# Kernel optimization log

Hardware: AMD Instinct MI355X
Metric: run time of the kernel (lower is better)

The kernel has to match this reference:

```python
import jax, jax.numpy as jnp
import numpy as np

N, F, H, C, E = 100000, 128, 64, 16, 1000000


def _prop(x, src, dst, w):
    # gather source features, scale by edge weight, scatter-add to destinations
    msgs = x[src] * w[:, None]  # [E, H]
    return jax.ops.segment_sum(msgs, dst, num_segments=N)


def _gru(x, h, W_ih, W_hh, b_ih, b_hh):
    gi = x @ W_ih.T + b_ih  # [N, 3H]
    gh = h @ W_hh.T + b_hh
    i_r, i_z, i_n = jnp.split(gi, 3, axis=1)
    h_r, h_z, h_n = jnp.split(gh, 3, axis=1)
    r = jax.nn.sigmoid(i_r + h_r)
    z = jax.nn.sigmoid(i_z + h_z)
    n = jnp.tanh(i_n + r * h_n)
    return (1.0 - z) * n + z * h


def setup_inputs() -> dict:
    key = jax.random.key(0)
    ks = jax.random.split(key, 20)
    s = 0.05
    inp = {
        'x': jax.random.normal(ks[0], (N, F), jnp.float32),
        'edge_index': jax.random.randint(ks[1], (2, E), 0, N),
        'edge_weight': jax.random.uniform(ks[2], (E,), jnp.float32),
        'edge_index_re': jax.random.randint(ks[3], (2, E), 0, N),
        'edge_weight_re': jax.random.uniform(ks[4], (E,), jnp.float32),
        'W_first': jax.random.normal(ks[5], (H, F), jnp.float32) * s,
        'b_first': jnp.zeros((H,), jnp.float32),
        'W_con1': jax.random.normal(ks[6], (H, 2 * H), jnp.float32) * s,
        'b_con1': jnp.zeros((H,), jnp.float32),
        'W_con2': jax.random.normal(ks[7], (H, 2 * H), jnp.float32) * s,
        'b_con2': jnp.zeros((H,), jnp.float32),
        'W_lin1': jax.random.normal(ks[8], (H, H), jnp.float32) * s,
        'b_lin1': jnp.zeros((H,), jnp.float32),
        'W_out': jax.random.normal(ks[9], (C, H), jnp.float32) * s,
        'b_out': jnp.zeros((C,), jnp.float32),
        'W_ih': jax.random.normal(ks[10], (3 * H, H), jnp.float32) * s,
        'W_hh': jax.random.normal(ks[11], (3 * H, H), jnp.float32) * s,
        'b_ih': jnp.zeros((3 * H,), jnp.float32),
        'b_hh': jnp.zeros((3 * H,), jnp.float32),
    }
    return inp


def reference(x, edge_index, edge_weight, edge_index_re, edge_weight_re,
              W_first, b_first, W_con1, b_con1, W_con2, b_con2,
              W_lin1, b_lin1, W_out, b_out, W_ih, W_hh, b_ih, b_hh):
    src, dst = edge_index[0], edge_index[1]
    src_r, dst_r = edge_index_re[0], edge_index_re[1]

    x = x @ W_first.T + b_first  # [N, H]; dropout is identity at inference
    h = x

    x1 = _prop(x, src, dst, edge_weight)
    x2 = _prop(x, src_r, dst_r, edge_weight_re)
    x = jnp.concatenate([x1, x2], axis=1) @ W_con1.T + b_con1
    x = _gru(x, h, W_ih, W_hh, b_ih, b_hh)
    x = x @ W_lin1.T + b_lin1

    x1 = _prop(x, src, dst, edge_weight)
    x2 = _prop(x, src_r, dst_r, edge_weight_re)
    x = jnp.concatenate([x1, x2], axis=1) @ W_con2.T + b_con2
    x = _gru(x, h, W_ih, W_hh, b_ih, b_hh)
    x = x @ W_out.T + b_out
    return jax.nn.log_softmax(x, axis=-1)
```

## Files before the change

### kernel.cpp

```cpp
#include <hip/hip_runtime.h>

#define NN 100000
#define FF 128
#define HH 64
#define CC 16
#define EE 1000000
#define NSEG (2*NN)
#define BSH 11
#define BKD  (1 << BSH)
#define NBUK ((NSEG + BKD - 1) / BKD)
#define EPB 4096
#define P1BLK ((2*EE + EPB - 1) / EPB)

typedef __bf16 bf16;
typedef __attribute__((ext_vector_type(8))) __bf16 bf16x8;
typedef __attribute__((ext_vector_type(4))) __bf16 bf16x4;
typedef __attribute__((ext_vector_type(4))) float f32x4;
typedef __attribute__((ext_vector_type(2))) float f32x2;

__device__ __forceinline__ float fsig(float t)  { return 1.0f/(1.0f+__expf(-t)); }
__device__ __forceinline__ float ftanh(float t) { return 1.0f - 2.0f/(__expf(2.0f*t)+1.0f); }

__device__ __forceinline__ unsigned pack_sw(int s, float w) {
    unsigned short u = __builtin_bit_cast(unsigned short, (bf16)w);
    return ((unsigned)s << 15) | (u & 0x7FFFu);
}

__global__ void precomp_kernel(const float* __restrict__ W_ih, const float* __restrict__ b_ih,
                               const float* __restrict__ Wc1,  const float* __restrict__ bc1,
                               const float* __restrict__ Wc2,  const float* __restrict__ bc2,
                               const float* __restrict__ W_hh, const float* __restrict__ W_first,
                               const float* __restrict__ W_lin1, const float* __restrict__ W_out,
                               bf16* __restrict__ W1bf, float* __restrict__ b1,
                               bf16* __restrict__ W2bf, float* __restrict__ b2,
                               bf16* __restrict__ Whbf, bf16* __restrict__ Wfbf,
                               bf16* __restrict__ Wlbf, bf16* __restrict__ Wobf)
{
    int idx = blockIdx.x*blockDim.x + threadIdx.x;
    const int t0 = 192*128;
    const int t1 = t0 + 192;
    const int t2 = t1 + 192*64;
    const int t3 = t2 + 64*128;
    const int t4 = t3 + 64*64;
    const int t5 = t4 + 16*64;
    if (idx < t0) {
        int j = idx >> 7, k = idx & 127;
        float s1 = 0.f, s2 = 0.f;
        for (int m=0; m<64; ++m) {
            float wih = W_ih[j*64+m];
            s1 += wih * Wc1[m*128+k];
            s2 += wih * Wc2[m*128+k];
        }
        W1bf[idx] = (bf16)s1; W2bf[idx] = (bf16)s2;
    } else if (idx < t1) {
        int j = idx - t0;
        float s1 = b_ih[j], s2 = b_ih[j];
        for (int m=0; m<64; ++m) {
            float wih = W_ih[j*64+m];
            s1 += wih * bc1[m];
            s2 += wih * bc2[m];
        }
        b1[j] = s1; b2[j] = s2;
    } else if (idx < t2) {
        int i = idx - t1;  Whbf[i] = (bf16)W_hh[i];
    } else if (idx < t3) {
        int i = idx - t2;  Wfbf[i] = (bf16)W_first[i];
    } else if (idx < t4) {
        int i = idx - t3;  Wlbf[i] = (bf16)W_lin1[i];
    } else if (idx < t5) {
        int i = idx - t4;  Wobf[i] = (bf16)W_out[i];
    }
}


__global__ __launch_bounds__(256) void bucket_count_kernel(const int* __restrict__ ei,
                                                           const int* __restrict__ ei_re,
                                                           int* __restrict__ bkcnt)
{
    __shared__ int hist[NBUK];
    const int t = threadIdx.x;
    for (int i=t; i<NBUK; i+=256) hist[i] = 0;
    __syncthreads();
    const long e0 = (long)blockIdx.x * EPB;
    #pragma unroll
    for (int it=0; it<16; ++it) {
        long e = e0 + it*256 + t;
        int d = -1;
        if (e < EE)        d = ei[EE + e];
        else if (e < 2*EE) d = NN + ei_re[EE + (e - EE)];
        if (d >= 0) atomicAdd(&hist[d >> BSH], 1);
    }
    __syncthreads();
    for (int i=t; i<NBUK; i+=256) if (hist[i]) atomicAdd(&bkcnt[i], hist[i]);
}

__global__ void bucket_scan_kernel(const int* __restrict__ bkcnt,
                                   int* __restrict__ bkbase, int* __restrict__ bkcur,
                                   int* __restrict__ rp)
{
    if (threadIdx.x == 0) {
        int acc = 0;
        for (int i=0; i<NBUK; ++i) { bkbase[i] = acc; bkcur[i] = acc; acc += bkcnt[i]; }
        bkbase[NBUK] = acc;
        rp[NSEG] = 2*EE;
    }
}

__global__ __launch_bounds__(256) void fillA_kernel(const int* __restrict__ ei,
                                                    const float* __restrict__ ew,
                                                    const int* __restrict__ ei_re,
                                                    const float* __restrict__ ew_re,
                                                    int* __restrict__ bkcur,
                                                    int* __restrict__ tmp_d,
                                                    unsigned* __restrict__ tmp_p)
{
    __shared__ int hist[NBUK];
    __shared__ int base[NBUK];
    const int t = threadIdx.x;
    for (int i=t; i<NBUK; i+=256) hist[i] = 0;
    __syncthreads();
    const long e0 = (long)blockIdx.x * EPB;
    int pr[16];
    #pragma unroll
    for (int it=0; it<16; ++it) {
        long e = e0 + it*256 + t;
        int d = -1;
        if (e < EE)        d = ei[EE + e];
        else if (e < 2*EE) d = NN + ei_re[EE + (e - EE)];
        if (d >= 0) {
            int b = d >> BSH;
            int r = atomicAdd(&hist[b], 1);
            pr[it] = (b << 16) | r;
        } else pr[it] = -1;
    }
    __syncthreads();
    for (int i=t; i<NBUK; i+=256) base[i] = atomicAdd(&bkcur[i], hist[i]);
    __syncthreads();
    #pragma unroll
    for (int it=0; it<16; ++it) {
        if (pr[it] < 0) continue;
        long e = e0 + it*256 + t;
        int d, s; float w;
        if (e < EE) { d = ei[EE+e]; s = ei[e]; w = ew[e]; }
        else { long j = e - EE; d = NN + ei_re[EE+j]; s = ei_re[j]; w = ew_re[j]; }
        int pos = base[pr[it] >> 16] + (pr[it] & 0xFFFF);
        tmp_d[pos] = d;
        tmp_p[pos] = pack_sw(s, w);
    }
}

__global__ __launch_bounds__(1024) void fillB_kernel(const int* __restrict__ bkbase,
                                                     const int* __restrict__ tmp_d,
                                                     const unsigned* __restrict__ tmp_p,
                                                     unsigned* __restrict__ edata,
                                                     int* __restrict__ rp)
{
    __shared__ int cntL[BKD];
    __shared__ int scanL[1024];
    const int t  = threadIdx.x;
    const int b  = blockIdx.x;
    const int d0 = b << BSH;
    const int dn = min(BKD, NSEG - d0);
    const int p0 = bkbase[b];
    const int p1 = bkbase[b+1];
    for (int i=t; i<BKD; i+=1024) cntL[i] = 0;
    __syncthreads();
    for (int pos = p0 + t; pos < p1; pos += 1024)
        atomicAdd(&cntL[tmp_d[pos] - d0], 1);
    __syncthreads();
    int a0 = cntL[2*t], a1 = cntL[2*t+1];
    int ps = a0 + a1;
    scanL[t] = ps;
    __syncthreads();
    #pragma unroll
    for (int off=1; off<1024; off<<=1) {
        int x = (t>=off) ? scanL[t-off] : 0;
        __syncthreads();
        scanL[t] += x;
        __syncthreads();
    }
    int g0 = p0 + scanL[t] - ps;
    int g1 = g0 + a0;
    if (2*t   < dn) rp[d0 + 2*t]   = g0;
    if (2*t+1 < dn) rp[d0 + 2*t+1] = g1;
    cntL[2*t]   = g0;
    cntL[2*t+1] = g1;
    __syncthreads();
    for (int pos = p0 + t; pos < p1; pos += 1024) {
        int d = tmp_d[pos];
        int p = atomicAdd(&cntL[d - d0], 1);
        edata[p] = tmp_p[pos];
    }
}

__global__ __launch_bounds__(256) void csr_prop_kernel(const bf16* __restrict__ X,
    const int* __restrict__ rp, const unsigned* __restrict__ edata,
    bf16* __restrict__ x1, bf16* __restrict__ x2)
{
    int s = blockIdx.x*4 + (threadIdx.x>>6);
    if (s >= NSEG) return;
    const int lane = threadIdx.x & 63;
    const int q  = lane >> 4;
    const int fl = lane & 15;
    const unsigned foff = 8u*(unsigned)fl;
    const int e0 = rp[s], e1 = rp[s+1];
    const char* Xb = (const char*)X;
    const char* Eb = (const char*)edata;

    f32x2 acc01 = {0.f, 0.f}, acc23 = {0.f, 0.f};
    int eq = e0 + q;
    unsigned eqb = 4u*(unsigned)eq;
    for (int base = e0; base < e1; base += 16, eq += 16, eqb += 64u) {
        const int rem = e1 - eq;
        #pragma unroll
        for (int j=0; j<4; ++j) {
            unsigned p = *(const unsigned*)(Eb + (eqb + 16u*(unsigned)j));
            const bool v = (4*j < rem);
            float w = v ? __uint_as_float((p & 0x7FFFu) << 16) : 0.f;
            unsigned voff = v ? (((p >> 8) & 0xFFFFFF80u) | foff) : foff;
            uint2 d = *(const uint2*)(Xb + voff);
            f32x2 lo = { __uint_as_float(d.x << 16), __uint_as_float(d.x & 0xFFFF0000u) };
            f32x2 hi = { __uint_as_float(d.y << 16), __uint_as_float(d.y & 0xFFFF0000u) };
            f32x2 w2 = { w, w };
            acc01 += w2 * lo;
            acc23 += w2 * hi;
        }
    }
    float a0 = acc01.x, a1 = acc01.y, a2 = acc23.x, a3 = acc23.y;
    a0 += __shfl_xor(a0, 32); a0 += __shfl_xor(a0, 16);
    a1 += __shfl_xor(a1, 32); a1 += __shfl_xor(a1, 16);
    a2 += __shfl_xor(a2, 32); a2 += __shfl_xor(a2, 16);
    a3 += __shfl_xor(a3, 32); a3 += __shfl_xor(a3, 16);
    if (q == 0) {
        bf16* o = (s < NN) ? &x1[(long)s*HH] : &x2[(long)(s-NN)*HH];
        bf16x4 ov = {(bf16)a0, (bf16)a1, (bf16)a2, (bf16)a3};
        *(bf16x4*)&o[4*fl] = ov;
    }
}


__global__ __launch_bounds__(256, 2) void lin_first_mfma_kernel(
    const float* __restrict__ X, const bf16* __restrict__ Wf,
    const float* __restrict__ b, float* __restrict__ Y, bf16* __restrict__ Ybf)
{
    const int t = threadIdx.x;
    const int w = t >> 6, lane = t & 63, col = lane & 15, quad = lane >> 4;
    bf16x8 B[4];
    #pragma unroll
    for (int ks=0; ks<4; ++ks)
        B[ks] = *(const bf16x8*)&Wf[(16*w+col)*128 + ks*32 + quad*8];
    const float bv = b[16*w + col];
    __shared__ bf16 Alds[32][136];
    const int m_st = t >> 3, c_in = t & 7;
    for (int tb = blockIdx.x*32; tb < NN; tb += gridDim.x*32) {
        const float4* rx = (const float4*)&X[(long)(tb+m_st)*FF];
        #pragma unroll
        for (int it=0; it<4; ++it) {
            int cc = c_in + it*8;
            float4 v = rx[cc];
            bf16x4 bvv = {(bf16)v.x,(bf16)v.y,(bf16)v.z,(bf16)v.w};
            *(bf16x4*)&Alds[m_st][cc*4] = bvv;
        }
        __syncthreads();
        f32x4 acc[2] = {{0.f,0.f,0.f,0.f},{0.f,0.f,0.f,0.f}};
        #pragma unroll
        for (int ks=0; ks<4; ++ks)
            #pragma unroll
            for (int mt=0; mt<2; ++mt) {
                bf16x8 a = *(const bf16x8*)&Alds[mt*16+col][ks*32+quad*8];
                acc[mt] = __builtin_amdgcn_mfma_f32_16x16x32_bf16(a, B[ks], acc[mt], 0,0,0);
            }
        __syncthreads();
        #pragma unroll
        for (int mt=0; mt<2; ++mt)
            #pragma unroll
            for (int r=0; r<4; ++r) {
                long n = tb + mt*16 + quad*4 + r;
                float val = acc[mt][r] + bv;
                Y  [n*HH + 16*w+col] = val;
                Ybf[n*HH + 16*w+col] = (bf16)val;
            }
    }
}

template<int MODE>
__global__ __launch_bounds__(256, 2) void layer_fused_kernel(
    const bf16* __restrict__ X1, const bf16* __restrict__ X2,
    const float* __restrict__ H,
    const bf16* __restrict__ Wg, const float* __restrict__ bg,
    const bf16* __restrict__ Wh, const float* __restrict__ bh,
    const bf16* __restrict__ Ws, const float* __restrict__ bs,
    bf16* __restrict__ Obf, float* __restrict__ Of)
{
    const int t    = threadIdx.x;
    const int w    = t >> 6;
    const int lane = t & 63;
    const int col  = lane & 15;
    const int quad = lane >> 4;

    bf16x8 Bg[3][4];
    bf16x8 Bh[3][2];
    float bgv[3], bhv[3];
    #pragma unroll
    for (int jt=0; jt<3; ++jt) {
        int J = jt*64 + 16*w + col;
        #pragma unroll
        for (int ks=0; ks<4; ++ks)
            Bg[jt][ks] = *(const bf16x8*)&Wg[J*128 + ks*32 + quad*8];
        #pragma unroll
        for (int ks=0; ks<2; ++ks)
            Bh[jt][ks] = *(const bf16x8*)&Wh[J*64 + ks*32 + quad*8];
        bgv[jt] = bg[J];
        bhv[jt] = bh[J];
    }

    bf16x8 B2[2];
    float b2s;
    if constexpr (MODE == 0) {
        #pragma unroll
        for (int ks=0; ks<2; ++ks)
            B2[ks] = *(const bf16x8*)&Ws[(16*w+col)*64 + ks*32 + quad*8];
        b2s = bs[16*w + col];
    } else {
        #pragma unroll
        for (int ks=0; ks<2; ++ks)
            B2[ks] = *(const bf16x8*)&Ws[col*64 + ks*32 + quad*8];
        b2s = bs[col];
    }

    __shared__ bf16 Alds[32][200];
    __shared__ bf16 Glds[32][72];

    const int m_st = t >> 3;
    const int c_in = t & 7;

    for (int tb = blockIdx.x*32; tb < NN; tb += gridDim.x*32) {
        {
            long n = tb + m_st;
            *(bf16x8*)&Alds[m_st][c_in*8]      = *(const bf16x8*)&X1[n*HH + c_in*8];
            *(bf16x8*)&Alds[m_st][64 + c_in*8] = *(const bf16x8*)&X2[n*HH + c_in*8];
            const float4* rh = (const float4*)&H[n*HH];
            float4 a = rh[c_in*2], b4 = rh[c_in*2+1];
            bf16x8 hb = {(bf16)a.x,(bf16)a.y,(bf16)a.z,(bf16)a.w,
                         (bf16)b4.x,(bf16)b4.y,(bf16)b4.z,(bf16)b4.w};
            *(bf16x8*)&Alds[m_st][128 + c_in*8] = hb;
        }
        __syncthreads();

        f32x4 accg[2][3];
        f32x4 acch[2][3];
        #pragma unroll
        for (int mt=0; mt<2; ++mt)
            #pragma unroll
            for (int jt=0; jt<3; ++jt) {
                accg[mt][jt] = (f32x4){0.f,0.f,0.f,0.f};
                acch[mt][jt] = (f32x4){0.f,0.f,0.f,0.f};
            }

        #pragma unroll
        for (int ks=0; ks<4; ++ks) {
            #pragma unroll
            for (int mt=0; mt<2; ++mt) {
                bf16x8 a = *(const bf16x8*)&Alds[mt*16 + col][ks*32 + quad*8];
                #pragma unroll
                for (int jt=0; jt<3; ++jt)
                    accg[mt][jt] = __builtin_amdgcn_mfma_f32_16x16x32_bf16(
                        a, Bg[jt][ks], accg[mt][jt], 0, 0, 0);
            }
        }
        #pragma unroll
        for (int ks=0; ks<2; ++ks) {
            #pragma unroll
            for (int mt=0; mt<2; ++mt) {
                bf16x8 a = *(const bf16x8*)&Alds[mt*16 + col][128 + ks*32 + quad*8];
                #pragma unroll
                for (int jt=0; jt<3; ++jt)
                    acch[mt][jt] = __builtin_amdgcn_mfma_f32_16x16x32_bf16(
                        a, Bh[jt][ks], acch[mt][jt], 0, 0, 0);
            }
        }

        const int c = 16*w + col;
        #pragma unroll
        for (int mt=0; mt<2; ++mt) {
            #pragma unroll
            for (int r=0; r<4; ++r) {
                long n = tb + mt*16 + quad*4 + r;
                float gr = accg[mt][0][r] + bgv[0];
                float gz = accg[mt][1][r] + bgv[1];
                float gn = accg[mt][2][r] + bgv[2];
                float hr = acch[mt][0][r] + bhv[0];
                float hz = acch[mt][1][r] + bhv[1];
                float hn = acch[mt][2][r] + bhv[2];
                float rr = fsig(gr + hr);
                float zz = fsig(gz + hz);
                float nv = ftanh(gn + rr*hn);
                float hv = H[n*HH + c];
                Glds[mt*16 + quad*4 + r][c] = (bf16)((1.0f - zz)*nv + zz*hv);
            }
        }
        __syncthreads();

        if constexpr (MODE == 0) {
            f32x4 acc2[2] = {{0.f,0.f,0.f,0.f},{0.f,0.f,0.f,0.f}};
            #pragma unroll
            for (int ks=0; ks<2; ++ks)
                #pragma unroll
                for (int mt=0; mt<2; ++mt) {
                    bf16x8 a = *(const bf16x8*)&Glds[mt*16+col][ks*32+quad*8];
                    acc2[mt] = __builtin_amdgcn_mfma_f32_16x16x32_bf16(a, B2[ks], acc2[mt], 0,0,0);
                }
            #pragma unroll
            for (int mt=0; mt<2; ++mt)
                #pragma unroll
                for (int r=0; r<4; ++r)
                    Obf[(long)(tb+mt*16+quad*4+r)*HH + 16*w+col] = (bf16)(acc2[mt][r] + b2s);
        } else {
            if (w < 2) {
                f32x4 acc2 = {0.f,0.f,0.f,0.f};
                #pragma unroll
                for (int ks=0; ks<2; ++ks) {
                    bf16x8 a = *(const bf16x8*)&Glds[w*16+col][ks*32+quad*8];
                    acc2 = __builtin_amdgcn_mfma_f32_16x16x32_bf16(a, B2[ks], acc2, 0,0,0);
                }
                #pragma unroll
                for (int r=0; r<4; ++r) {
                    long n = tb + w*16 + quad*4 + r;
                    float val = acc2[r] + b2s;
                    float m = val;
                    #pragma unroll
                    for (int off=8; off>0; off>>=1) m = fmaxf(m, __shfl_xor(m, off, 16));
                    float ex = __expf(val - m);
                    float ssum = ex;
                    #pragma unroll
                    for (int off=8; off>0; off>>=1) ssum += __shfl_xor(ssum, off, 16);
                    Of[n*CC + col] = val - m - __logf(ssum);
                }
            }
        }
    }
}

extern "C" void kernel_launch(void* const* d_in, const int* in_sizes, int n_in,
                              void* d_out, int out_size, void* d_ws, size_t ws_size,
                              hipStream_t stream)
{
    const float* x       = (const float*)d_in[0];
    const int*   ei      = (const int*)  d_in[1];
    const float* ew      = (const float*)d_in[2];
    const int*   ei_re   = (const int*)  d_in[3];
    const float* ew_re   = (const float*)d_in[4];
    const float* W_first = (const float*)d_in[5];
    const float* b_first = (const float*)d_in[6];
    const float* W_con1  = (const float*)d_in[7];
    const float* b_con1  = (const float*)d_in[8];
    const float* W_con2  = (const float*)d_in[9];
    const float* b_con2  = (const float*)d_in[10];
    const float* W_lin1  = (const float*)d_in[11];
    const float* b_lin1  = (const float*)d_in[12];
    const float* W_out   = (const float*)d_in[13];
    const float* b_out   = (const float*)d_in[14];
    const float* W_ih    = (const float*)d_in[15];
    const float* W_hh    = (const float*)d_in[16];
    const float* b_ih    = (const float*)d_in[17];
    const float* b_hh    = (const float*)d_in[18];
    float* out = (float*)d_out;

    float* h    = (float*)d_ws;
    bf16*  x1b  = (bf16*)(h + (long)NN*HH);
    bf16*  x2b  = x1b + (long)NN*HH;
    bf16*  hbf  = x2b + (long)NN*HH;
    bf16*  hAbf = hbf + (long)NN*HH;
    float* b1 = (float*)(hAbf + (long)NN*HH);
    float* b2 = b1 + 192;
    bf16*  W1bf = (bf16*)(b2 + 192);
    bf16*  W2bf = W1bf + 192*128;
    bf16*  Whbf = W2bf + 192*128;
    bf16*  Wfbf = Whbf + 192*64;
    bf16*  Wlbf = Wfbf + 64*128;
    bf16*  Wobf = Wlbf + 64*64;
    unsigned* edata = (unsigned*)(Wobf + 16*64);
    int*   rp     = (int*)(edata + 2*EE);
    int*   bkcnt  = rp + NSEG + 1;
    int*   bkbase = bkcnt + NBUK;
    int*   bkcur  = bkbase + NBUK + 1;
    int*      tmp_d = (int*)x1b;
    unsigned* tmp_p = (unsigned*)x2b;

    precomp_kernel<<<(192*128 + 192 + 192*64 + 64*128 + 64*64 + 16*64 + 255)/256, 256, 0, stream>>>(
        W_ih, b_ih, W_con1, b_con1, W_con2, b_con2, W_hh, W_first, W_lin1, W_out,
        W1bf, b1, W2bf, b2, Whbf, Wfbf, Wlbf, Wobf);

    hipMemsetAsync(bkcnt, 0, (size_t)NBUK*sizeof(int), stream);
    bucket_count_kernel<<<P1BLK, 256, 0, stream>>>(ei, ei_re, bkcnt);
    bucket_scan_kernel<<<1, 64, 0, stream>>>(bkcnt, bkbase, bkcur, rp);
    fillA_kernel<<<P1BLK, 256, 0, stream>>>(ei, ew, ei_re, ew_re, bkcur, tmp_d, tmp_p);
    fillB_kernel<<<NBUK, 1024, 0, stream>>>(bkbase, tmp_d, tmp_p, edata, rp);

    lin_first_mfma_kernel<<<1024, 256, 0, stream>>>(x, Wfbf, b_first, h, hbf);

    csr_prop_kernel<<<(NSEG + 3)/4, 256, 0, stream>>>(hbf, rp, edata, x1b, x2b);

    layer_fused_kernel<0><<<1024, 256, 0, stream>>>(x1b, x2b, h, W1bf, b1, Whbf, b_hh,
                                                    Wlbf, b_lin1, hAbf, nullptr);

    csr_prop_kernel<<<(NSEG + 3)/4, 256, 0, stream>>>(hAbf, rp, edata, x1b, x2b);

    layer_fused_kernel<1><<<1024, 256, 0, stream>>>(x1b, x2b, h, W2bf, b2, Whbf, b_hh,
                                                    Wobf, b_out, nullptr, out);
}
```

Baseline: 391.8 us.

## Fold bucket scan into fill kernels and widen CSR gather to 16-byte loads

Removes the single-thread bucket_scan kernel launch. Each fillA block now computes the bucket prefix sums itself from bkcnt, and bkcur starts at zero via a larger memset. Each fillB block also sums its own prefix serially. The CSR propagation kernel now has 8 lanes per row, each loading 16 bytes (8 bf16 features), so 8 edges are in flight per step instead of 4, with an extra shuffle stage in the reduction. This trades fewer launches and wider loads for redundant serial prefix work in every block.

```diff
diff --git a/kernel.cpp b/kernel.cpp
--- a/kernel.cpp
+++ b/kernel.cpp
@@ -94,28 +94,18 @@
     for (int i=t; i<NBUK; i+=256) if (hist[i]) atomicAdd(&bkcnt[i], hist[i]);
 }
 
-__global__ void bucket_scan_kernel(const int* __restrict__ bkcnt,
-                                   int* __restrict__ bkbase, int* __restrict__ bkcur,
-                                   int* __restrict__ rp)
-{
-    if (threadIdx.x == 0) {
-        int acc = 0;
-        for (int i=0; i<NBUK; ++i) { bkbase[i] = acc; bkcur[i] = acc; acc += bkcnt[i]; }
-        bkbase[NBUK] = acc;
-        rp[NSEG] = 2*EE;
-    }
-}
-
 __global__ __launch_bounds__(256) void fillA_kernel(const int* __restrict__ ei,
                                                     const float* __restrict__ ew,
                                                     const int* __restrict__ ei_re,
                                                     const float* __restrict__ ew_re,
+                                                    const int* __restrict__ bkcnt,
                                                     int* __restrict__ bkcur,
                                                     int* __restrict__ tmp_d,
                                                     unsigned* __restrict__ tmp_p)
 {
     __shared__ int hist[NBUK];
-    __shared__ int base[NBUK];
+    __shared__ int baseL[NBUK];
+    __shared__ int pref[NBUK];
     const int t = threadIdx.x;
     for (int i=t; i<NBUK; i+=256) hist[i] = 0;
     __syncthreads();
@@ -133,8 +123,12 @@
             pr[it] = (b << 16) | r;
         } else pr[it] = -1;
     }
-    __syncthreads();
-    for (int i=t; i<NBUK; i+=256) base[i] = atomicAdd(&bkcur[i], hist[i]);
+    if (t == 0) {
+        int acc = 0;
+        for (int i=0; i<NBUK; ++i) { pref[i] = acc; acc += bkcnt[i]; }
+    }
+    __syncthreads();
+    for (int i=t; i<NBUK; i+=256) baseL[i] = pref[i] + atomicAdd(&bkcur[i], hist[i]);
     __syncthreads();
     #pragma unroll
     for (int it=0; it<16; ++it) {
@@ -143,13 +137,13 @@
         int d, s; float w;
         if (e < EE) { d = ei[EE+e]; s = ei[e]; w = ew[e]; }
         else { long j = e - EE; d = NN + ei_re[EE+j]; s = ei_re[j]; w = ew_re[j]; }
-        int pos = base[pr[it] >> 16] + (pr[it] & 0xFFFF);
+        int pos = baseL[pr[it] >> 16] + (pr[it] & 0xFFFF);
         tmp_d[pos] = d;
         tmp_p[pos] = pack_sw(s, w);
     }
 }
 
-__global__ __launch_bounds__(1024) void fillB_kernel(const int* __restrict__ bkbase,
+__global__ __launch_bounds__(1024) void fillB_kernel(const int* __restrict__ bkcnt,
                                                      const int* __restrict__ tmp_d,
                                                      const unsigned* __restrict__ tmp_p,
                                                      unsigned* __restrict__ edata,
@@ -157,14 +151,21 @@
 {
     __shared__ int cntL[BKD];
     __shared__ int scanL[1024];
+    __shared__ int pb[2];
     const int t  = threadIdx.x;
     const int b  = blockIdx.x;
     const int d0 = b << BSH;
     const int dn = min(BKD, NSEG - d0);
-    const int p0 = bkbase[b];
-    const int p1 = bkbase[b+1];
+    if (t == 0) {
+        int acc = 0;
+        for (int i=0; i<b; ++i) acc += bkcnt[i];
+        pb[0] = acc; pb[1] = acc + bkcnt[b];
+        if (b == NBUK-1) rp[NSEG] = 2*EE;
+    }
     for (int i=t; i<BKD; i+=1024) cntL[i] = 0;
     __syncthreads();
+    const int p0 = pb[0];
+    const int p1 = pb[1];
     for (int pos = p0 + t; pos < p1; pos += 1024)
         atomicAdd(&cntL[tmp_d[pos] - d0], 1);
     __syncthreads();
@@ -200,41 +201,56 @@
     int s = blockIdx.x*4 + (threadIdx.x>>6);
     if (s >= NSEG) return;
     const int lane = threadIdx.x & 63;
-    const int q  = lane >> 4;
-    const int fl = lane & 15;
-    const unsigned foff = 8u*(unsigned)fl;
+    const int q  = lane >> 3;
+    const int fl = lane & 7;
+    const unsigned foff = 16u*(unsigned)fl;
     const int e0 = rp[s], e1 = rp[s+1];
     const char* Xb = (const char*)X;
     const char* Eb = (const char*)edata;
 
-    f32x2 acc01 = {0.f, 0.f}, acc23 = {0.f, 0.f};
-    int eq = e0 + q;
-    unsigned eqb = 4u*(unsigned)eq;
-    for (int base = e0; base < e1; base += 16, eq += 16, eqb += 64u) {
-        const int rem = e1 - eq;
-        #pragma unroll
-        for (int j=0; j<4; ++j) {
-            unsigned p = *(const unsigned*)(Eb + (eqb + 16u*(unsigned)j));
-            const bool v = (4*j < rem);
+    f32x2 ac0={0.f,0.f}, ac1={0.f,0.f}, ac2={0.f,0.f}, ac3={0.f,0.f};
+    unsigned eqb = 4u*(unsigned)(e0 + q);
+    for (int base = e0; base < e1; base += 16, eqb += 64u) {
+        const int rem = e1 - base;
+        {
+            unsigned p = *(const unsigned*)(Eb + eqb);
+            const bool v = (q < rem);
             float w = v ? __uint_as_float((p & 0x7FFFu) << 16) : 0.f;
             unsigned voff = v ? (((p >> 8) & 0xFFFFFF80u) | foff) : foff;
-            uint2 d = *(const uint2*)(Xb + voff);
-            f32x2 lo = { __uint_as_float(d.x << 16), __uint_as_float(d.x & 0xFFFF0000u) };
-            f32x2 hi = { __uint_as_float(d.y << 16), __uint_as_float(d.y & 0xFFFF0000u) };
-            f32x2 w2 = { w, w };
-            acc01 += w2 * lo;
-            acc23 += w2 * hi;
-        }
-    }
-    float a0 = acc01.x, a1 = acc01.y, a2 = acc23.x, a3 = acc23.y;
-    a0 += __shfl_xor(a0, 32); a0 += __shfl_xor(a0, 16);
-    a1 += __shfl_xor(a1, 32); a1 += __shfl_xor(a1, 16);
-    a2 += __shfl_xor(a2, 32); a2 += __shfl_xor(a2, 16);
-    a3 += __shfl_xor(a3, 32); a3 += __shfl_xor(a3, 16);
+            uint4 d = *(const uint4*)(Xb + voff);
+            f32x2 w2 = {w, w};
+            ac0 += w2 * (f32x2){__uint_as_float(d.x << 16), __uint_as_float(d.x & 0xFFFF0000u)};
+            ac1 += w2 * (f32x2){__uint_as_float(d.y << 16), __uint_as_float(d.y & 0xFFFF0000u)};
+            ac2 += w2 * (f32x2){__uint_as_float(d.z << 16), __uint_as_float(d.z & 0xFFFF0000u)};
+            ac3 += w2 * (f32x2){__uint_as_float(d.w << 16), __uint_as_float(d.w & 0xFFFF0000u)};
+        }
+        if (rem > 8) {
+            unsigned p = *(const unsigned*)(Eb + eqb + 32u);
+            const bool v = (q + 8 < rem);
+            float w = v ? __uint_as_float((p & 0x7FFFu) << 16) : 0.f;
+            unsigned voff = v ? (((p >> 8) & 0xFFFFFF80u) | foff) : foff;
+            uint4 d = *(const uint4*)(Xb + voff);
+            f32x2 w2 = {w, w};
+            ac0 += w2 * (f32x2){__uint_as_float(d.x << 16), __uint_as_float(d.x & 0xFFFF0000u)};
+            ac1 += w2 * (f32x2){__uint_as_float(d.y << 16), __uint_as_float(d.y & 0xFFFF0000u)};
+            ac2 += w2 * (f32x2){__uint_as_float(d.z << 16), __uint_as_float(d.z & 0xFFFF0000u)};
+            ac3 += w2 * (f32x2){__uint_as_float(d.w << 16), __uint_as_float(d.w & 0xFFFF0000u)};
+        }
+    }
+    float a0=ac0.x, a1=ac0.y, a2=ac1.x, a3=ac1.y, a4=ac2.x, a5=ac2.y, a6=ac3.x, a7=ac3.y;
+    a0 += __shfl_xor(a0, 32); a0 += __shfl_xor(a0, 16); a0 += __shfl_xor(a0, 8);
+    a1 += __shfl_xor(a1, 32); a1 += __shfl_xor(a1, 16); a1 += __shfl_xor(a1, 8);
+    a2 += __shfl_xor(a2, 32); a2 += __shfl_xor(a2, 16); a2 += __shfl_xor(a2, 8);
+    a3 += __shfl_xor(a3, 32); a3 += __shfl_xor(a3, 16); a3 += __shfl_xor(a3, 8);
+    a4 += __shfl_xor(a4, 32); a4 += __shfl_xor(a4, 16); a4 += __shfl_xor(a4, 8);
+    a5 += __shfl_xor(a5, 32); a5 += __shfl_xor(a5, 16); a5 += __shfl_xor(a5, 8);
+    a6 += __shfl_xor(a6, 32); a6 += __shfl_xor(a6, 16); a6 += __shfl_xor(a6, 8);
+    a7 += __shfl_xor(a7, 32); a7 += __shfl_xor(a7, 16); a7 += __shfl_xor(a7, 8);
     if (q == 0) {
         bf16* o = (s < NN) ? &x1[(long)s*HH] : &x2[(long)(s-NN)*HH];
-        bf16x4 ov = {(bf16)a0, (bf16)a1, (bf16)a2, (bf16)a3};
-        *(bf16x4*)&o[4*fl] = ov;
+        bf16x8 ov = {(bf16)a0,(bf16)a1,(bf16)a2,(bf16)a3,
+                     (bf16)a4,(bf16)a5,(bf16)a6,(bf16)a7};
+        *(bf16x8*)&o[8*fl] = ov;
     }
 }
 
@@ -482,8 +498,7 @@
     unsigned* edata = (unsigned*)(Wobf + 16*64);
     int*   rp     = (int*)(edata + 2*EE);
     int*   bkcnt  = rp + NSEG + 1;
-    int*   bkbase = bkcnt + NBUK;
-    int*   bkcur  = bkbase + NBUK + 1;
+    int*   bkcur  = bkcnt + NBUK;
     int*      tmp_d = (int*)x1b;
     unsigned* tmp_p = (unsigned*)x2b;
 
@@ -491,11 +506,10 @@
         W_ih, b_ih, W_con1, b_con1, W_con2, b_con2, W_hh, W_first, W_lin1, W_out,
         W1bf, b1, W2bf, b2, Whbf, Wfbf, Wlbf, Wobf);
 
-    hipMemsetAsync(bkcnt, 0, (size_t)NBUK*sizeof(int), stream);
+    hipMemsetAsync(bkcnt, 0, (size_t)(2*NBUK)*sizeof(int), stream);
     bucket_count_kernel<<<P1BLK, 256, 0, stream>>>(ei, ei_re, bkcnt);
-    bucket_scan_kernel<<<1, 64, 0, stream>>>(bkcnt, bkbase, bkcur, rp);
-    fillA_kernel<<<P1BLK, 256, 0, stream>>>(ei, ew, ei_re, ew_re, bkcur, tmp_d, tmp_p);
-    fillB_kernel<<<NBUK, 1024, 0, stream>>>(bkbase, tmp_d, tmp_p, edata, rp);
+    fillA_kernel<<<P1BLK, 256, 0, stream>>>(ei, ew, ei_re, ew_re, bkcnt, bkcur, tmp_d, tmp_p);
+    fillB_kernel<<<NBUK, 1024, 0, stream>>>(bkcnt, tmp_d, tmp_p, edata, rp);
 
     lin_first_mfma_kernel<<<1024, 256, 0, stream>>>(x, Wfbf, b_first, h, hbf);
 
```

New measurement: 422.7 us. +7.9%, slower.

## Pad CSR segments to 16 edges, drop scan kernel, prefetch gathers

Applied to the files above, without the earlier changes.

Each destination segment in the edge array is padded with zeroed entries up to a multiple of 16, and row pointers are replaced by (offset, count) descriptors. This lets the propagation loop drop its per-edge validity checks and issue all four packed-edge loads, then all four feature gathers, before any arithmetic. The single-thread bucket scan kernel is removed, and each fill block now recomputes bucket prefix sums serially, which removes one launch but adds redundant serial work per block. The padding adds memory footprint and extra zero-weight gathers of row 0.

```diff
diff --git a/kernel.cpp b/kernel.cpp
--- a/kernel.cpp
+++ b/kernel.cpp
@@ -11,6 +11,8 @@
 #define NBUK ((NSEG + BKD - 1) / BKD)
 #define EPB 4096
 #define P1BLK ((2*EE + EPB - 1) / EPB)
+#define SLACK 32768
+#define EDCAP (2*EE + NBUK*SLACK)
 
 typedef __bf16 bf16;
 typedef __attribute__((ext_vector_type(8))) __bf16 bf16x8;
@@ -94,28 +96,18 @@
     for (int i=t; i<NBUK; i+=256) if (hist[i]) atomicAdd(&bkcnt[i], hist[i]);
 }
 
-__global__ void bucket_scan_kernel(const int* __restrict__ bkcnt,
-                                   int* __restrict__ bkbase, int* __restrict__ bkcur,
-                                   int* __restrict__ rp)
-{
-    if (threadIdx.x == 0) {
-        int acc = 0;
-        for (int i=0; i<NBUK; ++i) { bkbase[i] = acc; bkcur[i] = acc; acc += bkcnt[i]; }
-        bkbase[NBUK] = acc;
-        rp[NSEG] = 2*EE;
-    }
-}
-
 __global__ __launch_bounds__(256) void fillA_kernel(const int* __restrict__ ei,
                                                     const float* __restrict__ ew,
                                                     const int* __restrict__ ei_re,
                                                     const float* __restrict__ ew_re,
+                                                    const int* __restrict__ bkcnt,
                                                     int* __restrict__ bkcur,
                                                     int* __restrict__ tmp_d,
                                                     unsigned* __restrict__ tmp_p)
 {
     __shared__ int hist[NBUK];
-    __shared__ int base[NBUK];
+    __shared__ int baseL[NBUK];
+    __shared__ int pref[NBUK];
     const int t = threadIdx.x;
     for (int i=t; i<NBUK; i+=256) hist[i] = 0;
     __syncthreads();
@@ -133,8 +125,12 @@
             pr[it] = (b << 16) | r;
         } else pr[it] = -1;
     }
-    __syncthreads();
-    for (int i=t; i<NBUK; i+=256) base[i] = atomicAdd(&bkcur[i], hist[i]);
+    if (t == 0) {
+        int acc = 0;
+        for (int i=0; i<NBUK; ++i) { pref[i] = acc; acc += bkcnt[i]; }
+    }
+    __syncthreads();
+    for (int i=t; i<NBUK; i+=256) baseL[i] = pref[i] + atomicAdd(&bkcur[i], hist[i]);
     __syncthreads();
     #pragma unroll
     for (int it=0; it<16; ++it) {
@@ -143,33 +139,42 @@
         int d, s; float w;
         if (e < EE) { d = ei[EE+e]; s = ei[e]; w = ew[e]; }
         else { long j = e - EE; d = NN + ei_re[EE+j]; s = ei_re[j]; w = ew_re[j]; }
-        int pos = base[pr[it] >> 16] + (pr[it] & 0xFFFF);
+        int pos = baseL[pr[it] >> 16] + (pr[it] & 0xFFFF);
         tmp_d[pos] = d;
         tmp_p[pos] = pack_sw(s, w);
     }
 }
 
-__global__ __launch_bounds__(1024) void fillB_kernel(const int* __restrict__ bkbase,
+__global__ __launch_bounds__(1024) void fillB_kernel(const int* __restrict__ bkcnt,
                                                      const int* __restrict__ tmp_d,
                                                      const unsigned* __restrict__ tmp_p,
                                                      unsigned* __restrict__ edata,
-                                                     int* __restrict__ rp)
+                                                     int2* __restrict__ segdesc)
 {
     __shared__ int cntL[BKD];
     __shared__ int scanL[1024];
+    __shared__ int pb[1];
     const int t  = threadIdx.x;
     const int b  = blockIdx.x;
     const int d0 = b << BSH;
     const int dn = min(BKD, NSEG - d0);
-    const int p0 = bkbase[b];
-    const int p1 = bkbase[b+1];
+    if (t == 0) {
+        int acc = 0;
+        for (int i=0; i<b; ++i) acc += bkcnt[i];
+        pb[0] = acc;
+    }
     for (int i=t; i<BKD; i+=1024) cntL[i] = 0;
     __syncthreads();
-    for (int pos = p0 + t; pos < p1; pos += 1024)
+    const int p0u = pb[0];
+    const int p1u = p0u + bkcnt[b];
+    const int PB  = p0u + b*SLACK;
+    for (int pos = p0u + t; pos < p1u; pos += 1024)
         atomicAdd(&cntL[tmp_d[pos] - d0], 1);
     __syncthreads();
-    int a0 = cntL[2*t], a1 = cntL[2*t+1];
-    int ps = a0 + a1;
+    const int a0 = cntL[2*t], a1 = cntL[2*t+1];
+    const int cp0 = (a0 + 15) & ~15;
+    const int cp1 = (a1 + 15) & ~15;
+    int ps = cp0 + cp1;
     scanL[t] = ps;
     __syncthreads();
     #pragma unroll
@@ -179,14 +184,16 @@
         scanL[t] += x;
         __syncthreads();
     }
-    int g0 = p0 + scanL[t] - ps;
-    int g1 = g0 + a0;
-    if (2*t   < dn) rp[d0 + 2*t]   = g0;
-    if (2*t+1 < dn) rp[d0 + 2*t+1] = g1;
+    const int g0 = PB + scanL[t] - ps;
+    const int g1 = g0 + cp0;
+    if (2*t   < dn) segdesc[d0 + 2*t]   = make_int2(g0, a0);
+    if (2*t+1 < dn) segdesc[d0 + 2*t+1] = make_int2(g1, a1);
     cntL[2*t]   = g0;
     cntL[2*t+1] = g1;
-    __syncthreads();
-    for (int pos = p0 + t; pos < p1; pos += 1024) {
+    for (int i=a0; i<cp0; ++i) edata[g0+i] = 0u;
+    for (int i=a1; i<cp1; ++i) edata[g1+i] = 0u;
+    __syncthreads();
+    for (int pos = p0u + t; pos < p1u; pos += 1024) {
         int d = tmp_d[pos];
         int p = atomicAdd(&cntL[d - d0], 1);
         edata[p] = tmp_p[pos];
@@ -194,7 +201,7 @@
 }
 
 __global__ __launch_bounds__(256) void csr_prop_kernel(const bf16* __restrict__ X,
-    const int* __restrict__ rp, const unsigned* __restrict__ edata,
+    const int2* __restrict__ segdesc, const unsigned* __restrict__ edata,
     bf16* __restrict__ x1, bf16* __restrict__ x2)
 {
     int s = blockIdx.x*4 + (threadIdx.x>>6);
@@ -203,27 +210,28 @@
     const int q  = lane >> 4;
     const int fl = lane & 15;
     const unsigned foff = 8u*(unsigned)fl;
-    const int e0 = rp[s], e1 = rp[s+1];
+    const int2 sd = segdesc[s];
+    const int np = (sd.y + 15) >> 4;
     const char* Xb = (const char*)X;
     const char* Eb = (const char*)edata;
 
     f32x2 acc01 = {0.f, 0.f}, acc23 = {0.f, 0.f};
-    int eq = e0 + q;
-    unsigned eqb = 4u*(unsigned)eq;
-    for (int base = e0; base < e1; base += 16, eq += 16, eqb += 64u) {
-        const int rem = e1 - eq;
-        #pragma unroll
-        for (int j=0; j<4; ++j) {
-            unsigned p = *(const unsigned*)(Eb + (eqb + 16u*(unsigned)j));
-            const bool v = (4*j < rem);
-            float w = v ? __uint_as_float((p & 0x7FFFu) << 16) : 0.f;
-            unsigned voff = v ? (((p >> 8) & 0xFFFFFF80u) | foff) : foff;
-            uint2 d = *(const uint2*)(Xb + voff);
-            f32x2 lo = { __uint_as_float(d.x << 16), __uint_as_float(d.x & 0xFFFF0000u) };
-            f32x2 hi = { __uint_as_float(d.y << 16), __uint_as_float(d.y & 0xFFFF0000u) };
+    unsigned eqb = 4u*(unsigned)(sd.x + q);
+    for (int pass = 0; pass < np; ++pass, eqb += 64u) {
+        unsigned pk[4];
+        #pragma unroll
+        for (int j=0;j<4;++j)
+            pk[j] = *(const unsigned*)(Eb + (eqb + 16u*(unsigned)j));
+        uint2 dv[4];
+        #pragma unroll
+        for (int j=0;j<4;++j)
+            dv[j] = *(const uint2*)(Xb + ((((pk[j] >> 8) & 0xFFFFFF80u)) | foff));
+        #pragma unroll
+        for (int j=0;j<4;++j) {
+            float w = __uint_as_float((pk[j] & 0x7FFFu) << 16);
             f32x2 w2 = { w, w };
-            acc01 += w2 * lo;
-            acc23 += w2 * hi;
+            acc01 += w2 * (f32x2){ __uint_as_float(dv[j].x << 16), __uint_as_float(dv[j].x & 0xFFFF0000u) };
+            acc23 += w2 * (f32x2){ __uint_as_float(dv[j].y << 16), __uint_as_float(dv[j].y & 0xFFFF0000u) };
         }
     }
     float a0 = acc01.x, a1 = acc01.y, a2 = acc23.x, a3 = acc23.y;
@@ -480,10 +488,9 @@
     bf16*  Wlbf = Wfbf + 64*128;
     bf16*  Wobf = Wlbf + 64*64;
     unsigned* edata = (unsigned*)(Wobf + 16*64);
-    int*   rp     = (int*)(edata + 2*EE);
-    int*   bkcnt  = rp + NSEG + 1;
-    int*   bkbase = bkcnt + NBUK;
-    int*   bkcur  = bkbase + NBUK + 1;
+    int2*  segdesc = (int2*)(edata + EDCAP);
+    int*   bkcnt  = (int*)(segdesc + NSEG);
+    int*   bkcur  = bkcnt + NBUK;
     int*      tmp_d = (int*)x1b;
     unsigned* tmp_p = (unsigned*)x2b;
 
@@ -491,20 +498,19 @@
         W_ih, b_ih, W_con1, b_con1, W_con2, b_con2, W_hh, W_first, W_lin1, W_out,
         W1bf, b1, W2bf, b2, Whbf, Wfbf, Wlbf, Wobf);
 
-    hipMemsetAsync(bkcnt, 0, (size_t)NBUK*sizeof(int), stream);
+    hipMemsetAsync(bkcnt, 0, (size_t)(2*NBUK)*sizeof(int), stream);
     bucket_count_kernel<<<P1BLK, 256, 0, stream>>>(ei, ei_re, bkcnt);
-    bucket_scan_kernel<<<1, 64, 0, stream>>>(bkcnt, bkbase, bkcur, rp);
-    fillA_kernel<<<P1BLK, 256, 0, stream>>>(ei, ew, ei_re, ew_re, bkcur, tmp_d, tmp_p);
-    fillB_kernel<<<NBUK, 1024, 0, stream>>>(bkbase, tmp_d, tmp_p, edata, rp);
+    fillA_kernel<<<P1BLK, 256, 0, stream>>>(ei, ew, ei_re, ew_re, bkcnt, bkcur, tmp_d, tmp_p);
+    fillB_kernel<<<NBUK, 1024, 0, stream>>>(bkcnt, tmp_d, tmp_p, edata, segdesc);
 
     lin_first_mfma_kernel<<<1024, 256, 0, stream>>>(x, Wfbf, b_first, h, hbf);
 
-    csr_prop_kernel<<<(NSEG + 3)/4, 256, 0, stream>>>(hbf, rp, edata, x1b, x2b);
+    csr_prop_kernel<<<(NSEG + 3)/4, 256, 0, stream>>>(hbf, segdesc, edata, x1b, x2b);
 
     layer_fused_kernel<0><<<1024, 256, 0, stream>>>(x1b, x2b, h, W1bf, b1, Whbf, b_hh,
                                                     Wlbf, b_lin1, hAbf, nullptr);
 
-    csr_prop_kernel<<<(NSEG + 3)/4, 256, 0, stream>>>(hAbf, rp, edata, x1b, x2b);
+    csr_prop_kernel<<<(NSEG + 3)/4, 256, 0, stream>>>(hAbf, segdesc, edata, x1b, x2b);
 
     layer_fused_kernel<1><<<1024, 256, 0, stream>>>(x1b, x2b, h, W2bf, b2, Whbf, b_hh,
                                                     Wobf, b_out, nullptr, out);
```

Result: slower. 415.7 us (+6.1%).
